# Optimization experiments

Hardware: AMD Instinct MI355X
Metric: run time of the kernel (lower is better)

The kernel has to match this reference:

```python
import jax, jax.numpy as jnp
import numpy as np

N_NODES = 100000
N_EDGES = 1600000
D_IN, D_HID, D_OUT = 64, 64, 2


def setup_inputs() -> dict:
    key = jax.random.key(0)
    k1, k2, k3, k4 = jax.random.split(key, 4)
    x = jax.random.normal(k1, (N_NODES, D_IN), dtype=jnp.float32)
    edge_index = jax.random.randint(k2, (2, N_EDGES), 0, N_NODES, dtype=jnp.int64)
    W1 = jax.random.normal(k3, (D_IN, D_HID), dtype=jnp.float32) * (1.0 / np.sqrt(D_IN))
    b1 = jnp.zeros((D_HID,), dtype=jnp.float32)
    W2 = jax.random.normal(k4, (D_HID, D_OUT), dtype=jnp.float32) * (1.0 / np.sqrt(D_HID))
    b2 = jnp.zeros((D_OUT,), dtype=jnp.float32)
    return {"x": x, "edge_index": edge_index, "W1": W1, "b1": b1, "W2": W2, "b2": b2}


def _gcn_norm(edge_index, num_nodes):
    # PyG GCNConv default: add self-loops, symmetric normalization D^-1/2 (A+I) D^-1/2
    loops = jnp.arange(num_nodes, dtype=edge_index.dtype)
    row = jnp.concatenate([edge_index[0], loops])  # source
    col = jnp.concatenate([edge_index[1], loops])  # destination
    deg = jax.ops.segment_sum(jnp.ones_like(col, dtype=jnp.float32), col, num_segments=num_nodes)
    dinv = jnp.where(deg > 0, jax.lax.rsqrt(deg), 0.0)
    norm = dinv[row] * dinv[col]  # [E + N]
    return row, col, norm


def _gcn_conv(x, W, b, row, col, norm, num_nodes):
    h = x @ W                              # [N, D_out] small GEMM first (PyG order)
    msg = h[row] * norm[:, None]           # gather + scale  [E+N, D_out]
    out = jax.ops.segment_sum(msg, col, num_segments=num_nodes)  # scatter-add
    return out + b


def reference(x, edge_index, W1, b1, W2, b2):
    n = x.shape[0]
    row, col, norm = _gcn_norm(edge_index, n)
    h = jax.nn.relu(_gcn_conv(x, W1, b1, row, col, norm, n))
    return _gcn_conv(h, W2, b2, row, col, norm, n)
```

## Files before the change

### kernel.cpp

```cpp
#include <hip/hip_runtime.h>


#define D_IN 64
#define NBBITS 8
#define NBK_PAD 512
#define BSTRIDE 16
#define PCH 4096
#define NWV 8
#define SCAP 5120
#define RPB 10

typedef __attribute__((ext_vector_type(8))) short bf16x8;
typedef __attribute__((ext_vector_type(4))) float f32x4;

__device__ __forceinline__ float b2f(unsigned short u) {
    unsigned v = ((unsigned)u) << 16;
    float f;
    __builtin_memcpy(&f, &v, 4);
    return f;
}
__device__ __forceinline__ unsigned short f2b(float f) {
    unsigned u;
    __builtin_memcpy(&u, &f, 4);
    u += 0x7FFFu + ((u >> 16) & 1u);
    return (unsigned short)(u >> 16);
}

__device__ __forceinline__ void acc8(float* a, uint4 rv, float wgt) {
    a[0] = fmaf(wgt, b2f((unsigned short)(rv.x & 0xFFFFu)), a[0]);
    a[1] = fmaf(wgt, b2f((unsigned short)(rv.x >> 16)), a[1]);
    a[2] = fmaf(wgt, b2f((unsigned short)(rv.y & 0xFFFFu)), a[2]);
    a[3] = fmaf(wgt, b2f((unsigned short)(rv.y >> 16)), a[3]);
    a[4] = fmaf(wgt, b2f((unsigned short)(rv.z & 0xFFFFu)), a[4]);
    a[5] = fmaf(wgt, b2f((unsigned short)(rv.z >> 16)), a[5]);
    a[6] = fmaf(wgt, b2f((unsigned short)(rv.w & 0xFFFFu)), a[6]);
    a[7] = fmaf(wgt, b2f((unsigned short)(rv.w >> 16)), a[7]);
}

__global__ __launch_bounds__(512, 8) void k_part_gemm(
        const int* __restrict__ ep, int* __restrict__ bptr,
        unsigned* __restrict__ ebuf,
        const float* __restrict__ x, const float* __restrict__ W,
        unsigned short* __restrict__ H, int E, int N, int nPart, int nGemm) {
    __shared__ __align__(16) char smraw[39040];
    int tid = threadIdx.x;
    int lane = tid & 63;
    int wv = tid >> 6;

    if (blockIdx.x < nPart) {
        int* whist = (int*)smraw;
        int* lofs  = whist + NWV * NBK_PAD;
        int* hcnt  = lofs + NBK_PAD;
        int* gbase = hcnt + NBK_PAD;
        int* fsh   = gbase + NBK_PAD;
        unsigned* stage = (unsigned*)(fsh + 16);

        for (int i = tid; i < NWV * NBK_PAD; i += 512) whist[i] = 0;
        if (tid < 64) {
            int bad = 0;
            for (int i = tid; i < 1024; i += 64)
                if (ep[2 * i + 1] != 0) bad = 1;
            unsigned long long m = __ballot(bad);
            if (tid == 0) fsh[0] = (m == 0ull) ? 1 : 0;
        }
        __syncthreads();
        int f = fsh[0];
        long base = (long)blockIdx.x * PCH;
        long rem64 = (long)E - base;
        int nE = rem64 > PCH ? PCH : (int)rem64;
        int j0 = tid * 8;
        int nv = nE - j0;
        nv = nv < 0 ? 0 : (nv > 8 ? 8 : nv);
        unsigned cc[8], rr2[8];
        #pragma unroll
        for (int k = 0; k < 8; ++k) { cc[k] = 0; rr2[k] = 0; }
        bool fullv = (nv == 8);
        const uint4* p4 = (const uint4*)ep;
        if (f) {
            if (fullv && ((E & 1) == 0)) {
                size_t cb = ((size_t)E + (size_t)base + j0) >> 1;
                uint4 a0 = p4[cb + 0], a1 = p4[cb + 1];
                uint4 a2 = p4[cb + 2], a3 = p4[cb + 3];
                cc[0] = a0.x; cc[1] = a0.z; cc[2] = a1.x; cc[3] = a1.z;
                cc[4] = a2.x; cc[5] = a2.z; cc[6] = a3.x; cc[7] = a3.z;
            } else {
                for (int k = 0; k < 8; ++k)
                    if (k < nv) cc[k] = (unsigned)ep[2 * ((size_t)E + base + j0 + k)];
            }
        } else {
            if (fullv && ((E & 3) == 0)) {
                size_t cb = ((size_t)E + (size_t)base + j0) >> 2;
                uint4 a0 = p4[cb + 0], a1 = p4[cb + 1];
                cc[0] = a0.x; cc[1] = a0.y; cc[2] = a0.z; cc[3] = a0.w;
                cc[4] = a1.x; cc[5] = a1.y; cc[6] = a1.z; cc[7] = a1.w;
            } else {
                for (int k = 0; k < 8; ++k)
                    if (k < nv) cc[k] = (unsigned)ep[(size_t)E + base + j0 + k];
            }
        }
        if (f) {
            if (fullv && ((E & 1) == 0)) {
                size_t rbb = ((size_t)base + j0) >> 1;
                uint4 b0 = p4[rbb + 0], b1 = p4[rbb + 1];
                uint4 b2 = p4[rbb + 2], b3 = p4[rbb + 3];
                rr2[0] = b0.x; rr2[1] = b0.z; rr2[2] = b1.x; rr2[3] = b1.z;
                rr2[4] = b2.x; rr2[5] = b2.z; rr2[6] = b3.x; rr2[7] = b3.z;
            } else {
                for (int k = 0; k < 8; ++k)
                    if (k < nv) rr2[k] = (unsigned)ep[2 * ((size_t)base + j0 + k)];
            }
        } else {
            if (fullv && ((E & 3) == 0)) {
                size_t rbb = ((size_t)base + j0) >> 2;
                uint4 b0 = p4[rbb + 0], b1 = p4[rbb + 1];
                rr2[0] = b0.x; rr2[1] = b0.y; rr2[2] = b0.z; rr2[3] = b0.w;
                rr2[4] = b1.x; rr2[5] = b1.y; rr2[6] = b1.z; rr2[7] = b1.w;
            } else {
                for (int k = 0; k < 8; ++k)
                    if (k < nv) rr2[k] = (unsigned)ep[(size_t)base + j0 + k];
            }
        }
        int* myh = whist + wv * NBK_PAD;
        #pragma unroll
        for (int k = 0; k < 8; ++k)
            if (k < nv) atomicAdd(&myh[cc[k] >> NBBITS], 1);
        __syncthreads();
        if (tid < NBK_PAD) {
            int run = 0;
            #pragma unroll
            for (int w = 0; w < NWV; ++w) {
                int v = whist[w * NBK_PAD + tid];
                whist[w * NBK_PAD + tid] = run;
                run += v;
            }
            hcnt[tid] = run;
            int s = run;
            #pragma unroll
            for (int off = 1; off < 64; off <<= 1) {
                int t2 = __shfl(s, lane - off);
                if (lane >= off) s += t2;
            }
            if (lane == 63) fsh[1 + (tid >> 6)] = s;
            lofs[tid] = s - run;
        }
        __syncthreads();
        if (tid < NBK_PAD) {
            int w8 = tid >> 6, add = 0;
            #pragma unroll
            for (int q = 0; q < NWV; ++q)
                if (q < w8) add += fsh[1 + q];
            lofs[tid] += add;
        }
        __syncthreads();
        for (int i = tid; i < NWV * NBK_PAD; i += 512)
            whist[i] += lofs[i & (NBK_PAD - 1)];
        __syncthreads();
        #pragma unroll
        for (int k = 0; k < 8; ++k) {
            if (k < nv) {
                unsigned c = cc[k];
                int b = c >> NBBITS;
                int pos = atomicAdd(&myh[b], 1);
                stage[pos] = rr2[k] | ((c & ((1u << NBBITS) - 1)) << 17);
            }
        }
        __syncthreads();
        if (tid < NBK_PAD && hcnt[tid])
            gbase[tid] = atomicAdd(&bptr[tid * BSTRIDE], hcnt[tid]);
        __syncthreads();
        for (int i = tid; i < nE; i += 512) {
            int lob = 0, hib = NBK_PAD;
            #pragma unroll
            for (int it = 0; it < 9; ++it) {
                int mid = (lob + hib) >> 1;
                if (lofs[mid] <= i) lob = mid; else hib = mid;
            }
            int b = lob;
            ebuf[(size_t)b * SCAP + gbase[b] + (i - lofs[b])] = stage[i];
        }
    } else {
        unsigned short* Wt = (unsigned short*)smraw;
        for (int i = tid; i < 64 * 64; i += 512) {
            int c = i & 63, k = i >> 6;
            Wt[c * 64 + k] = f2b(W[k * 64 + c]);
        }
        __syncthreads();
        int lm = lane & 15, lk = lane >> 4;
        int gwid = (blockIdx.x - nPart) * NWV + wv;
        int wstride = nGemm * NWV;
        int ntiles = (N + 15) >> 4;
        for (int tile = gwid; tile < ntiles; tile += wstride) {
            int rbase = tile << 4;
            int arow = rbase + lm;
            const float* xr = x + (size_t)(arow < N ? arow : N - 1) * 64;
            bf16x8 afrag[2];
            #pragma unroll
            for (int ks = 0; ks < 2; ++ks) {
                float4 u0 = *(const float4*)(xr + ks * 32 + lk * 8);
                float4 u1 = *(const float4*)(xr + ks * 32 + lk * 8 + 4);
                afrag[ks][0] = (short)f2b(u0.x); afrag[ks][1] = (short)f2b(u0.y);
                afrag[ks][2] = (short)f2b(u0.z); afrag[ks][3] = (short)f2b(u0.w);
                afrag[ks][4] = (short)f2b(u1.x); afrag[ks][5] = (short)f2b(u1.y);
                afrag[ks][6] = (short)f2b(u1.z); afrag[ks][7] = (short)f2b(u1.w);
            }
            f32x4 acc[4] = {{0.f, 0.f, 0.f, 0.f}, {0.f, 0.f, 0.f, 0.f},
                            {0.f, 0.f, 0.f, 0.f}, {0.f, 0.f, 0.f, 0.f}};
            #pragma unroll
            for (int ks = 0; ks < 2; ++ks)
                #pragma unroll
                for (int ct = 0; ct < 4; ++ct) {
                    bf16x8 bf = *(const bf16x8*)(Wt + (ct * 16 + lm) * 64
                                                 + ks * 32 + lk * 8);
                    acc[ct] = __builtin_amdgcn_mfma_f32_16x16x32_bf16(
                        afrag[ks], bf, acc[ct], 0, 0, 0);
                }
            #pragma unroll
            for (int ct = 0; ct < 4; ++ct)
                #pragma unroll
                for (int j = 0; j < 4; ++j) {
                    int row = rbase + lk * 4 + j;
                    if (row < N)
                        H[(size_t)row * 64 + ct * 16 + lm] = f2b(acc[ct][j]);
                }
        }
    }
}

__global__ __launch_bounds__(512, 8) void k_bucket(
        const unsigned* __restrict__ ebuf, const int* __restrict__ bptr,
        int* __restrict__ offs, float* __restrict__ dinv,
        int* __restrict__ srcA, int N, int E) {
    __shared__ int hist[256];
    __shared__ int escan[256];
    __shared__ int wsum[8];
    __shared__ int loSh;
    __shared__ int stage[SCAP];
    int tid = threadIdx.x, b = blockIdx.x;
    int lane = tid & 63, wid = tid >> 6;
    if (tid < 256) hist[tid] = 0;
    int cb = (tid < b) ? bptr[tid * BSTRIDE] : 0;
    #pragma unroll
    for (int off = 32; off > 0; off >>= 1) cb += __shfl_xor(cb, off);
    if (lane == 0) wsum[wid] = cb;
    if (tid == 0 && b == 0) offs[N] = E;
    __syncthreads();
    if (tid == 0) {
        int t = 0;
        #pragma unroll
        for (int q = 0; q < 8; ++q) t += wsum[q];
        loSh = t;
    }
    __syncthreads();
    int lo = loSh;
    int m = bptr[b * BSTRIDE];
    size_t rb = (size_t)b * SCAP;
    unsigned ew[RPB];
    #pragma unroll
    for (int k = 0; k < RPB; ++k) {
        int idx = tid + k * 512;
        ew[k] = (idx < m) ? ebuf[rb + idx] : 0xFFFFFFFFu;
    }
    #pragma unroll
    for (int k = 0; k < RPB; ++k)
        if (ew[k] != 0xFFFFFFFFu) atomicAdd(&hist[ew[k] >> 17], 1);
    __syncthreads();
    if (tid < 256) {
        int v = hist[tid], ss = v;
        #pragma unroll
        for (int off = 1; off < 64; off <<= 1) {
            int t2 = __shfl(ss, lane - off);
            if (lane >= off) ss += t2;
        }
        if (lane == 63) wsum[wid] = ss;
        escan[tid] = ss - v;
    }
    __syncthreads();
    if (tid < 256) {
        int w4 = tid >> 6, add = 0;
        #pragma unroll
        for (int q = 0; q < 4; ++q)
            if (q < w4) add += wsum[q];
        int ex = escan[tid] + add;
        escan[tid] = ex;
        int g = (b << NBBITS) + tid;
        if (g < N) {
            offs[g] = lo + ex;
            dinv[g] = rsqrtf((float)(hist[tid] + 1));
        }
    }
    __syncthreads();
    #pragma unroll
    for (int k = 0; k < RPB; ++k) {
        if (ew[k] != 0xFFFFFFFFu) {
            unsigned w = ew[k];
            int lc = w >> 17;
            int src = (int)(w & 0x1FFFFu);
            int sl = escan[lc] + atomicSub(&hist[lc], 1) - 1;
            if (sl < SCAP) stage[sl] = src;
            else srcA[lo + sl] = src;
        }
    }
    __syncthreads();
    int mm = min(m, SCAP);
    for (int i = tid; i < mm; i += 512) srcA[lo + i] = stage[i];
}

__global__ void k_agg1(const unsigned short* __restrict__ H1,
                       const int* __restrict__ srcA,
                       const float* __restrict__ dinv, const int* __restrict__ offs,
                       const float* __restrict__ b1, const float* __restrict__ W2,
                       float* __restrict__ Z, int N) {
    int wid = (blockIdx.x * blockDim.x + threadIdx.x) >> 6;
    int lane = threadIdx.x & 63;
    int g = lane >> 3, s = lane & 7;
    int n = wid * 8 + g;
    bool nvalid = (n < N);
    int nn = nvalid ? n : 0;
    float dn = dinv[nn];
    int base = offs[nn];
    int cnt = nvalid ? (offs[nn + 1] - base) : 0;
    int cm = cnt;
    #pragma unroll
    for (int off = 8; off <= 32; off <<= 1) cm = max(cm, __shfl_xor(cm, off));
    const uint4* H4 = (const uint4*)H1;
    uint4 rs = H4[(size_t)nn * 8 + s];
    float4 b1a = *(const float4*)(b1 + s * 8);
    float4 b1b = *(const float4*)(b1 + s * 8 + 4);
    const float4* w2p = (const float4*)(W2 + s * 16);
    float4 q0 = w2p[0], q1 = w2p[1], q2 = w2p[2], q3 = w2p[3];
    float a[8];
    #pragma unroll
    for (int k = 0; k < 8; ++k) a[k] = 0.f;
    int gb = g << 3;
    int sv = 0; float wl = 0.f;
    if (s < cnt) { sv = srcA[base + s]; wl = dinv[sv]; }
    for (int j0 = 0; j0 < cm; j0 += 8) {
        int svn = 0; float wln = 0.f;
        int jn = j0 + 8;
        if (jn + s < cnt) { svn = srcA[base + jn + s]; wln = dinv[svn]; }
        int   s0 = __shfl(sv, gb + 0), s1 = __shfl(sv, gb + 1);
        int   s2 = __shfl(sv, gb + 2), s3 = __shfl(sv, gb + 3);
        int   s4 = __shfl(sv, gb + 4), s5 = __shfl(sv, gb + 5);
        int   s6 = __shfl(sv, gb + 6), s7 = __shfl(sv, gb + 7);
        float w0 = __shfl(wl, gb + 0), w1 = __shfl(wl, gb + 1);
        float w2 = __shfl(wl, gb + 2), w3 = __shfl(wl, gb + 3);
        float w4 = __shfl(wl, gb + 4), w5 = __shfl(wl, gb + 5);
        float w6 = __shfl(wl, gb + 6), w7 = __shfl(wl, gb + 7);
        uint4 r0 = H4[(size_t)s0 * 8 + s];
        uint4 r1 = H4[(size_t)s1 * 8 + s];
        uint4 r2 = H4[(size_t)s2 * 8 + s];
        uint4 r3 = H4[(size_t)s3 * 8 + s];
        uint4 r4 = H4[(size_t)s4 * 8 + s];
        uint4 r5 = H4[(size_t)s5 * 8 + s];
        uint4 r6 = H4[(size_t)s6 * 8 + s];
        uint4 r7 = H4[(size_t)s7 * 8 + s];
        acc8(a, r0, w0); acc8(a, r1, w1); acc8(a, r2, w2); acc8(a, r3, w3);
        acc8(a, r4, w4); acc8(a, r5, w5); acc8(a, r6, w6); acc8(a, r7, w7);
        sv = svn; wl = wln;
    }
    acc8(a, rs, dn);
    float h0 = fmaxf(dn * a[0] + b1a.x, 0.f);
    float h1 = fmaxf(dn * a[1] + b1a.y, 0.f);
    float h2 = fmaxf(dn * a[2] + b1a.z, 0.f);
    float h3 = fmaxf(dn * a[3] + b1a.w, 0.f);
    float h4 = fmaxf(dn * a[4] + b1b.x, 0.f);
    float h5 = fmaxf(dn * a[5] + b1b.y, 0.f);
    float h6 = fmaxf(dn * a[6] + b1b.z, 0.f);
    float h7 = fmaxf(dn * a[7] + b1b.w, 0.f);
    float p0 = h0 * q0.x + h1 * q0.z + h2 * q1.x + h3 * q1.z
             + h4 * q2.x + h5 * q2.z + h6 * q3.x + h7 * q3.z;
    float p1 = h0 * q0.y + h1 * q0.w + h2 * q1.y + h3 * q1.w
             + h4 * q2.y + h5 * q2.w + h6 * q3.y + h7 * q3.w;
    #pragma unroll
    for (int off = 1; off < 8; off <<= 1) {
        p0 += __shfl_xor(p0, off);
        p1 += __shfl_xor(p1, off);
    }
    if (s == 0 && nvalid) { Z[n * 2 + 0] = p0; Z[n * 2 + 1] = p1; }
}

__global__ void k_agg2(const float* __restrict__ Z, const int* __restrict__ srcA,
                       const float* __restrict__ dinv, const int* __restrict__ offs,
                       const float* __restrict__ b2, float* __restrict__ out, int N) {
    int t = blockIdx.x * blockDim.x + threadIdx.x;
    int lane = threadIdx.x & 63;
    int n = (t >> 6) * 4 + (lane >> 4);
    int sl = lane & 15;
    if (n >= N) return;
    int base = offs[n];
    int cnt = offs[n + 1] - base;
    float a0 = 0.f, a1 = 0.f;
    const float2* Z2 = (const float2*)Z;
    for (int i = sl; i < cnt; i += 16) {
        int src = srcA[base + i];
        float w = dinv[src];
        float2 zv = Z2[src];
        a0 += w * zv.x;
        a1 += w * zv.y;
    }
    #pragma unroll
    for (int off = 8; off > 0; off >>= 1) {
        a0 += __shfl_xor(a0, off);
        a1 += __shfl_xor(a1, off);
    }
    if (sl == 0) {
        float dn = dinv[n];
        float2 zs = Z2[n];
        out[n * 2 + 0] = dn * (a0 + dn * zs.x) + b2[0];
        out[n * 2 + 1] = dn * (a1 + dn * zs.y) + b2[1];
    }
}

extern "C" void kernel_launch(void* const* d_in, const int* in_sizes, int n_in,
                              void* d_out, int out_size, void* d_ws, size_t ws_size,
                              hipStream_t stream) {
    const float* x  = (const float*)d_in[0];
    const int*   ep = (const int*)d_in[1];
    const float* W1 = (const float*)d_in[2];
    const float* b1 = (const float*)d_in[3];
    const float* W2 = (const float*)d_in[4];
    const float* b2 = (const float*)d_in[5];
    float* out = (float*)d_out;

    const int N = in_sizes[0] / D_IN;
    const int E = in_sizes[1] / 2;

    char* ws = (char*)d_ws;
    size_t o = 0;
    auto alloc = [&](size_t bytes) {
        size_t r = o;
        o = (o + bytes + 255) & ~(size_t)255;
        return r;
    };
    int*            bptr  = (int*)           (ws + alloc((size_t)NBK_PAD * BSTRIDE * 4));
    float*          dinv  = (float*)         (ws + alloc((size_t)N * 4));
    int*            offs  = (int*)           (ws + alloc((size_t)(N + 1) * 4));
    unsigned*       ebuf  = (unsigned*)      (ws + alloc((size_t)NBK_PAD * SCAP * 4));
    int*            srcA  = (int*)           (ws + alloc((size_t)E * 4));
    unsigned short* H1    = (unsigned short*)(ws + alloc((size_t)N * 64 * 2));
    float*          Z     = (float*)         (ws + alloc((size_t)N * 2 * 4));

    const int nbk = (N + (1 << NBBITS) - 1) >> NBBITS;
    const int nPart = (E + PCH - 1) / PCH;
    int nGemm = 1024 - nPart;
    if (nGemm < 64) nGemm = 64;

    (void)hipMemsetAsync(bptr, 0, (size_t)NBK_PAD * BSTRIDE * sizeof(int), stream);
    k_part_gemm<<<nPart + nGemm, 512, 0, stream>>>(ep, bptr, ebuf, x, W1, H1,
                                                   E, N, nPart, nGemm);
    k_bucket<<<nbk, 512, 0, stream>>>(ebuf, bptr, offs, dinv, srcA, N, E);
    int nwav = (N + 7) / 8;
    k_agg1<<<(nwav + 3) / 4, 256, 0, stream>>>(H1, srcA, dinv, offs, b1, W2, Z, N);
    k_agg2<<<(N + 15) / 16, 256, 0, stream>>>(Z, srcA, dinv, offs, b2, out, N);
}
```

Baseline: 88.61 us.

## Sort nodes by in-degree within buckets to balance agg1 wave work

k_bucket now builds a per-bucket counting sort of nodes by in-degree (capped at 63) and writes a permutation array. k_agg1 processes nodes in that permuted order, so the 8 nodes sharing a wavefront have similar edge counts and the max-degree loop wastes fewer lanes. The cost is extra shared-memory histogram and scan work in k_bucket, a permutation write and read, and less contiguous access to H1, dinv and offs in k_agg1.

```diff
diff --git a/kernel.cpp b/kernel.cpp
--- a/kernel.cpp
+++ b/kernel.cpp
@@ -229,9 +229,10 @@
 __global__ __launch_bounds__(512, 8) void k_bucket(
         const unsigned* __restrict__ ebuf, const int* __restrict__ bptr,
         int* __restrict__ offs, float* __restrict__ dinv,
-        int* __restrict__ srcA, int N, int E) {
+        int* __restrict__ srcA, int* __restrict__ perm, int N, int E) {
     __shared__ int hist[256];
     __shared__ int escan[256];
+    __shared__ int dhist[64];
     __shared__ int wsum[8];
     __shared__ int loSh;
     __shared__ int stage[SCAP];
@@ -273,6 +274,8 @@
         }
         if (lane == 63) wsum[wid] = ss;
         escan[tid] = ss - v;
+    } else if (tid < 320) {
+        dhist[tid - 256] = 0;
     }
     __syncthreads();
     if (tid < 256) {
@@ -287,6 +290,24 @@
             offs[g] = lo + ex;
             dinv[g] = rsqrtf((float)(hist[tid] + 1));
         }
+        atomicAdd(&dhist[min(hist[tid], 63)], 1);
+    }
+    __syncthreads();
+    if (tid < 64) {
+        int v = dhist[tid], ss = v;
+        #pragma unroll
+        for (int off = 1; off < 64; off <<= 1) {
+            int t2 = __shfl(ss, lane - off);
+            if (lane >= off) ss += t2;
+        }
+        dhist[tid] = ss - v;
+    }
+    __syncthreads();
+    if (tid < 256) {
+        int d = min(hist[tid], 63);
+        int rank = atomicAdd(&dhist[d], 1);
+        int g = (b << NBBITS) + tid;
+        perm[(b << NBBITS) + rank] = (g < N) ? g : -1;
     }
     __syncthreads();
     #pragma unroll
@@ -308,13 +329,15 @@
 __global__ void k_agg1(const unsigned short* __restrict__ H1,
                        const int* __restrict__ srcA,
                        const float* __restrict__ dinv, const int* __restrict__ offs,
+                       const int* __restrict__ perm,
                        const float* __restrict__ b1, const float* __restrict__ W2,
-                       float* __restrict__ Z, int N) {
+                       float* __restrict__ Z, int N, int nSlots) {
     int wid = (blockIdx.x * blockDim.x + threadIdx.x) >> 6;
     int lane = threadIdx.x & 63;
     int g = lane >> 3, s = lane & 7;
-    int n = wid * 8 + g;
-    bool nvalid = (n < N);
+    int slot = wid * 8 + g;
+    int n = (slot < nSlots) ? perm[slot] : -1;
+    bool nvalid = (n >= 0);
     int nn = nvalid ? n : 0;
     float dn = dinv[nn];
     int base = offs[nn];
@@ -432,15 +455,17 @@
         o = (o + bytes + 255) & ~(size_t)255;
         return r;
     };
+    const int nbk = (N + (1 << NBBITS) - 1) >> NBBITS;
+    const int nSlots = nbk << NBBITS;
     int*            bptr  = (int*)           (ws + alloc((size_t)NBK_PAD * BSTRIDE * 4));
     float*          dinv  = (float*)         (ws + alloc((size_t)N * 4));
     int*            offs  = (int*)           (ws + alloc((size_t)(N + 1) * 4));
+    int*            perm  = (int*)           (ws + alloc((size_t)nSlots * 4));
     unsigned*       ebuf  = (unsigned*)      (ws + alloc((size_t)NBK_PAD * SCAP * 4));
     int*            srcA  = (int*)           (ws + alloc((size_t)E * 4));
     unsigned short* H1    = (unsigned short*)(ws + alloc((size_t)N * 64 * 2));
     float*          Z     = (float*)         (ws + alloc((size_t)N * 2 * 4));
 
-    const int nbk = (N + (1 << NBBITS) - 1) >> NBBITS;
     const int nPart = (E + PCH - 1) / PCH;
     int nGemm = 1024 - nPart;
     if (nGemm < 64) nGemm = 64;
@@ -448,8 +473,9 @@
     (void)hipMemsetAsync(bptr, 0, (size_t)NBK_PAD * BSTRIDE * sizeof(int), stream);
     k_part_gemm<<<nPart + nGemm, 512, 0, stream>>>(ep, bptr, ebuf, x, W1, H1,
                                                    E, N, nPart, nGemm);
-    k_bucket<<<nbk, 512, 0, stream>>>(ebuf, bptr, offs, dinv, srcA, N, E);
-    int nwav = (N + 7) / 8;
-    k_agg1<<<(nwav + 3) / 4, 256, 0, stream>>>(H1, srcA, dinv, offs, b1, W2, Z, N);
+    k_bucket<<<nbk, 512, 0, stream>>>(ebuf, bptr, offs, dinv, srcA, perm, N, E);
+    int nwav = (nSlots + 7) / 8;
+    k_agg1<<<(nwav + 3) / 4, 256, 0, stream>>>(H1, srcA, dinv, offs, perm,
+                                               b1, W2, Z, N, nSlots);
     k_agg2<<<(N + 15) / 16, 256, 0, stream>>>(Z, srcA, dinv, offs, b2, out, N);
 }
```

Result: slower. 96.30 us (+8.7%).
